# Kernel optimization log

Measured on AMD Instinct MI355X. Metric: run time of the kernel, lower is better.

The kernel has to match this reference:

```python
import jax, jax.numpy as jnp
import numpy as np

D_MODEL = 1024
NUM_HEADS = 16
HEAD_DIM = D_MODEL // NUM_HEADS


def setup_inputs() -> dict:
    key = jax.random.key(0)
    ks = jax.random.split(key, 11)
    B, S = 2, 2048
    inp = {
        "query": jax.random.normal(ks[0], (B, S, D_MODEL), jnp.float32),
        "key": jax.random.normal(ks[1], (B, S, D_MODEL), jnp.float32),
        "value": jax.random.normal(ks[2], (B, S, D_MODEL), jnp.float32),
        "mask": 1,
        "w_q": jax.random.normal(ks[3], (D_MODEL, D_MODEL), jnp.float32) / np.sqrt(D_MODEL),
        "b_q": jax.random.normal(ks[4], (D_MODEL,), jnp.float32) * 0.02,
        "w_k": jax.random.normal(ks[5], (D_MODEL, D_MODEL), jnp.float32) / np.sqrt(D_MODEL),
        "b_k": jax.random.normal(ks[6], (D_MODEL,), jnp.float32) * 0.02,
        "w_v": jax.random.normal(ks[7], (D_MODEL, D_MODEL), jnp.float32) / np.sqrt(D_MODEL),
        "b_v": jax.random.normal(ks[8], (D_MODEL,), jnp.float32) * 0.02,
        "w_o": jax.random.normal(ks[9], (D_MODEL, D_MODEL), jnp.float32) / np.sqrt(D_MODEL),
        "b_o": jax.random.normal(ks[10], (D_MODEL,), jnp.float32) * 0.02,
    }
    return inp


def reference(query, key, value, mask, w_q, b_q, w_k, b_k, w_v, b_v, w_o, b_o):
    B, S, _ = query.shape
    H, Dh = NUM_HEADS, HEAD_DIM
    # projections (torch Linear: x @ W.T + b; here w_* stored as [in, out])
    q = (query @ w_q + b_q).reshape(B, S, H, Dh).transpose(0, 2, 1, 3)  # [B,H,S,Dh]
    k = (key @ w_k + b_k).reshape(B, S, H, Dh).transpose(0, 2, 1, 3)
    v = (value @ w_v + b_v).reshape(B, S, H, Dh).transpose(0, 2, 1, 3)
    scale = 1.0 / jnp.sqrt(jnp.asarray(Dh, q.dtype))
    scores = jnp.einsum("bhqd,bhkd->bhqk", q, k) * scale  # [B,H,S,S]
    if mask:
        causal = jnp.tril(jnp.ones((S, S), dtype=bool))
        scores = jnp.where(causal, scores, jnp.asarray(-1e9, scores.dtype))
    attn = jax.nn.softmax(scores, axis=-1)
    x = jnp.einsum("bhqk,bhkd->bhqd", attn, v)  # [B,H,S,Dh]
    x = x.transpose(0, 2, 1, 3).reshape(B, S, H * Dh)
    return x @ w_o + b_o
```

## Files before the change

### kernel.cpp

```cpp
#include <hip/hip_runtime.h>
#include <hip/hip_bf16.h>

using bf16 = __hip_bfloat16;

typedef __attribute__((ext_vector_type(4))) short short4v;
typedef __attribute__((ext_vector_type(8))) short short8v;
typedef __attribute__((ext_vector_type(4))) float f32x4;

static constexpr int D  = 1024;
static constexpr int H  = 16;
static constexpr int DH = 64;
static constexpr int B  = 2;
static constexpr int S  = 2048;
static constexpr int M  = B * S;
static constexpr size_t MD = (size_t)M * D;
static constexpr size_t WSZ = (size_t)D * D;

#define QS_CONST 0.18033688011112042f

__device__ __forceinline__ unsigned short f2b(float f) {
    union { float f; unsigned u; } v; v.f = f;
    return (unsigned short)((v.u + 0x7FFFu + ((v.u >> 16) & 1u)) >> 16);
}
__device__ __forceinline__ unsigned pkbf(float a, float b) {
    float2 t; t.x = a; t.y = b;
    __hip_bfloat162 h = __float22bfloat162_rn(t);
    union { __hip_bfloat162 h; unsigned u; } cv; cv.h = h;
    return cv.u;
}
__device__ __forceinline__ short8v pack8(short4v a, short4v b) {
    short8v r;
    r[0]=a[0]; r[1]=a[1]; r[2]=a[2]; r[3]=a[3];
    r[4]=b[0]; r[5]=b[1]; r[6]=b[2]; r[7]=b[3];
    return r;
}
__device__ __forceinline__ short8v ld_frag(const short* rowp, int lg) {
    short4v a = *reinterpret_cast<const short4v*>(rowp + 4*lg);
    short4v b = *reinterpret_cast<const short4v*>(rowp + 16 + 4*lg);
    return pack8(a, b);
}

__device__ __forceinline__ void gl_lds16(const void* g, void* l) {
    __builtin_amdgcn_global_load_lds(
        (const __attribute__((address_space(1))) unsigned int*)g,
        (__attribute__((address_space(3))) unsigned int*)l, 16, 0, 0);
}

__global__ __launch_bounds__(256) void cvt_all_kernel(
    const float* __restrict__ w0, const float* __restrict__ w1,
    const float* __restrict__ w2, const float* __restrict__ w3,
    unsigned short* __restrict__ t0, unsigned short* __restrict__ t1,
    unsigned short* __restrict__ t2, unsigned short* __restrict__ t3,
    const float* __restrict__ x0, const float* __restrict__ x1,
    const float* __restrict__ x2,
    unsigned short* __restrict__ y0, unsigned short* __restrict__ y1,
    unsigned short* __restrict__ y2)
{
    __shared__ float tile[32][33];
    const int z = blockIdx.z;
    if (z < 4) {
        const float* W = z==0 ? w0 : z==1 ? w1 : z==2 ? w2 : w3;
        unsigned short* T = z==0 ? t0 : z==1 ? t1 : z==2 ? t2 : t3;
        const int k0 = (blockIdx.x & 31) * 32, n0 = (blockIdx.x >> 5) * 32;
        const int t = threadIdx.x, r = t>>3, c4 = (t&7)*4;
        float4 v = *reinterpret_cast<const float4*>(&W[(size_t)(k0+r)*D + n0 + c4]);
        tile[r][c4+0]=v.x; tile[r][c4+1]=v.y; tile[r][c4+2]=v.z; tile[r][c4+3]=v.w;
        __syncthreads();
        uint2 p;
        p.x = pkbf(tile[c4+0][r], tile[c4+1][r]);
        p.y = pkbf(tile[c4+2][r], tile[c4+3][r]);
        *reinterpret_cast<uint2*>(T + (size_t)(n0+r)*D + k0 + c4) = p;
    } else {
        const float* X = z==4 ? x0 : z==5 ? x1 : x2;
        unsigned short* Y = z==4 ? y0 : z==5 ? y1 : y2;
        const size_t base = (size_t)blockIdx.x * 256 + threadIdx.x;
        const size_t stride = (size_t)1024 * 256;
#pragma unroll
        for (int j = 0; j < 4; ++j) {
            const size_t i = base + (size_t)j * stride;
            float4 f = reinterpret_cast<const float4*>(X)[i];
            uint2 p; p.x = pkbf(f.x, f.y); p.y = pkbf(f.z, f.w);
            reinterpret_cast<uint2*>(Y)[i] = p;
        }
    }
}

#define GEMM_CORE_LDS(XPTR, WPTR)                                              \
    __shared__ short As[2][128*32];                                            \
    __shared__ short Bs[2][128*32];                                            \
    const int tid = threadIdx.x;                                               \
    const int wid = tid>>6, lane = tid&63;                                     \
    const int wr = wid>>1, wc = wid&1;                                         \
    const int lg = lane>>4, lr = lane&15;                                      \
    const int qw = (lane&3) ^ ((lane>>3)&3);        \
    const int qr = lg ^ ((lr>>1)&3);                \
    f32x4 acc[4][4];                                                           \
    _Pragma("unroll")                                                          \
    for (int i=0;i<4;i++)                                                      \
        _Pragma("unroll")                                                      \
        for (int j=0;j<4;j++) acc[i][j] = f32x4{0.f,0.f,0.f,0.f};              \
    const int srow = (lane>>2);                                                \
    auto stage = [&](int buf, int k0) {                                        \
        _Pragma("unroll")                                                      \
        for (int c=0;c<2;c++) {                                                \
            const int r0 = 32*wid + 16*c;                                      \
            const int r  = r0 + srow;                                          \
            gl_lds16(XPTR + (size_t)(m0+r)*1024 + k0 + qw*8, &As[buf][r0*32]); \
            gl_lds16(WPTR + (size_t)(n0+r)*1024 + k0 + qw*8, &Bs[buf][r0*32]); \
        }                                                                      \
    };                                                                         \
    stage(0, 0);                                                               \
    int cur = 0;                                                               \
    for (int k0 = 0; k0 < 1024; k0 += 32) {                                    \
        __syncthreads();                     \
        if (k0 + 32 < 1024) stage(cur^1, k0 + 32);                             \
        short8v af[4], bfr[4];                                                 \
        _Pragma("unroll")                                                      \
        for (int i=0;i<4;i++) {                                                \
            const int R = wr*64 + i*16 + lr;                                   \
            af[i] = *reinterpret_cast<const short8v*>(&As[cur][R*32 + qr*8]);  \
        }                                                                      \
        _Pragma("unroll")                                                      \
        for (int j=0;j<4;j++) {                                                \
            const int R = wc*64 + j*16 + lr;                                   \
            bfr[j] = *reinterpret_cast<const short8v*>(&Bs[cur][R*32 + qr*8]); \
        }                                                                      \
        __builtin_amdgcn_s_setprio(1);                                         \
        _Pragma("unroll")                                                      \
        for (int i=0;i<4;i++)                                                  \
            _Pragma("unroll")                                                  \
            for (int j=0;j<4;j++)                                              \
                acc[i][j] = __builtin_amdgcn_mfma_f32_16x16x32_bf16(           \
                    af[i], bfr[j], acc[i][j], 0,0,0);                          \
        __builtin_amdgcn_s_setprio(0);                                         \
        cur ^= 1;                                                              \
    }

__global__ __launch_bounds__(256) void gemm_qkv_lds(
    const unsigned short* __restrict__ Xq, const unsigned short* __restrict__ Xk,
    const unsigned short* __restrict__ Xv, const unsigned short* __restrict__ WtBase,
    const float* __restrict__ bq, const float* __restrict__ bk,
    const float* __restrict__ bv, unsigned short* __restrict__ qkBase,
    unsigned short* __restrict__ va)
{
    const int z = blockIdx.z;
    const unsigned short* X = z==0 ? Xq : z==1 ? Xk : Xv;
    const unsigned short* Wt = WtBase + (size_t)z * WSZ;
    const float* bias = z==0 ? bq : z==1 ? bk : bv;
    const int m0 = blockIdx.x*128, n0 = blockIdx.y*128;

    GEMM_CORE_LDS(X, Wt)

#pragma unroll
    for (int i=0;i<4;i++) {
#pragma unroll
        for (int j=0;j<4;j++) {
            const int n = n0 + wc*64 + j*16 + lr;
            const float bv2 = bias[n];
#pragma unroll
            for (int r=0;r<4;r++) {
                const int m = m0 + wr*64 + i*16 + lg*4 + r;
                float v = acc[i][j][r] + bv2;
                const int bb=m>>11, ss=m&2047, hh=n>>6, dh=n&63;
                if (z == 0) {
                    v *= QS_CONST;
                    qkBase[(((size_t)(bb*H+hh))*S + ss)*DH + dh] = f2b(v);
                } else if (z == 1) {
                    (qkBase + MD)[(((size_t)(bb*H+hh))*S + ss)*DH + dh] = f2b(v);
                } else {
                    va[(((size_t)(bb*H+hh))*DH + dh)*S + ss] = f2b(v);
                }
            }
        }
    }
}

template<int OUTBF>
__global__ __launch_bounds__(256) void gemm_out_lds(
    const unsigned short* __restrict__ Xc, const unsigned short* __restrict__ Wt,
    const float* __restrict__ bias, void* __restrict__ Y)
{
    const int m0 = blockIdx.x*128, n0 = blockIdx.y*128;

    GEMM_CORE_LDS(Xc, Wt)

#pragma unroll
    for (int i=0;i<4;i++) {
#pragma unroll
        for (int j=0;j<4;j++) {
            const int n = n0 + wc*64 + j*16 + lr;
            const float bv = bias[n];
#pragma unroll
            for (int r=0;r<4;r++) {
                const int m = m0 + wr*64 + i*16 + lg*4 + r;
                const float v = acc[i][j][r] + bv;
                if (OUTBF) ((unsigned short*)Y)[(size_t)m*D + n] = f2b(v);
                else       ((float*)Y)[(size_t)m*D + n] = v;
            }
        }
    }
}

__global__ __launch_bounds__(256) void attn_mfma(
    const unsigned short* __restrict__ Qa,
    const unsigned short* __restrict__ Ka,
    const unsigned short* __restrict__ Va,
    unsigned short* __restrict__ Ctx)
{
    __shared__ short Ks[2][64*64];
    __shared__ short Vs[2][64*64];
    short (*Ob)[72] = (short(*)[72])Ks;

    const int tid = threadIdx.x;
    const int i   = blockIdx.x;
    const int xcd = i & 7;
    const int o   = i >> 3;
    const int bh  = (xcd << 2) + (o >> 5);
    const int qt  = ((o >> 5) & 1) ? (o & 31) : 31 - (o & 31);
    const int bb = bh>>4, hh = bh&15;
    const int q0 = qt*64;
    const int wid = tid>>6, lane = tid&63;
    const int lg = lane>>4, lr = lane&15;
    const size_t qkbase = (size_t)bh*S*DH;
    const size_t vbase  = (size_t)bh*DH*S;

    const int qrow = q0 + wid*16 + lr;
    short8v qf[2];
    {
        const unsigned short* qp = Qa + qkbase + (size_t)qrow*DH;
#pragma unroll
        for (int c=0;c<2;c++) {
            short4v a = *reinterpret_cast<const short4v*>(qp + 32*c + 4*lg);
            short4v b = *reinterpret_cast<const short4v*>(qp + 32*c + 16 + 4*lg);
            qf[c] = pack8(a, b);
        }
    }

    float lsum = 0.f;
    f32x4 oacc[4];
#pragma unroll
    for (int dt=0;dt<4;dt++) oacc[dt] = f32x4{0.f,0.f,0.f,0.f};

    const int srsub = lane >> 3;
    const int scol  = 8 * ((lane & 7) ^ srsub);

    auto stage = [&](int buf, int j0) {
#pragma unroll
        for (int c2=0;c2<2;c2++) {
            const int rb = 16*wid + 8*c2;
            gl_lds16(Ka + qkbase + (size_t)(j0 + rb + srsub)*DH + scol,
                     &Ks[buf][rb*64]);
            gl_lds16(Va + vbase  + (size_t)(rb + srsub)*S + j0 + scol,
                     &Vs[buf][rb*64]);
        }
    };

    const int r7 = lr & 7;
    const int l4 = 4*(lg & 1), g0 = lg >> 1;
    int offA[2], offB[2];
#pragma unroll
    for (int c=0;c<2;c++) {
        offA[c] = l4 + 8*((4*c + g0)     ^ r7);
        offB[c] = l4 + 8*((4*c + 2 + g0) ^ r7);
    }

    const int NT = qt + 1;
    stage(0, 0);
    for (int t = 0; t < NT; ++t) {
        const int j0 = t*64;
        const int cur = t & 1;
        __syncthreads();
        if (t + 1 < NT) stage(cur ^ 1, j0 + 64);

        __builtin_amdgcn_s_setprio(1);
        f32x4 st[4];
#pragma unroll
        for (int jt=0;jt<4;jt++) {
            f32x4 s = f32x4{0.f,0.f,0.f,0.f};
#pragma unroll
            for (int c=0;c<2;c++) {
                const short* rowp = &Ks[cur][(jt*16 + lr)*64];
                short4v a = *reinterpret_cast<const short4v*>(rowp + offA[c]);
                short4v b = *reinterpret_cast<const short4v*>(rowp + offB[c]);
                s = __builtin_amdgcn_mfma_f32_16x16x32_bf16(pack8(a,b), qf[c], s, 0,0,0);
            }
            st[jt] = s;
        }
        __builtin_amdgcn_s_setprio(0);

        float p[16];
        if (t == NT-1) {
#pragma unroll
            for (int jt=0;jt<4;jt++)
#pragma unroll
                for (int r=0;r<4;r++) {
                    const int j = j0 + jt*16 + lg*4 + r;
                    p[jt*4+r] = (j <= qrow) ? st[jt][r] : -1e30f;
                }
        } else {
#pragma unroll
            for (int jt=0;jt<4;jt++)
#pragma unroll
                for (int r=0;r<4;r++) p[jt*4+r] = st[jt][r];
        }
#pragma unroll
        for (int e=0;e<16;e++) { p[e] = exp2f(p[e]); lsum += p[e]; }

        uint4 u0, u1;
        u0.x = pkbf(p[0],p[1]);   u0.y = pkbf(p[2],p[3]);
        u0.z = pkbf(p[4],p[5]);   u0.w = pkbf(p[6],p[7]);
        u1.x = pkbf(p[8],p[9]);   u1.y = pkbf(p[10],p[11]);
        u1.z = pkbf(p[12],p[13]); u1.w = pkbf(p[14],p[15]);
        short8v pf0, pf1;
        *reinterpret_cast<uint4*>(&pf0) = u0;
        *reinterpret_cast<uint4*>(&pf1) = u1;

        __builtin_amdgcn_s_setprio(1);
#pragma unroll
        for (int dt=0;dt<4;dt++) {
            const short* rowp = &Vs[cur][(dt*16 + lr)*64];
            short4v a0 = *reinterpret_cast<const short4v*>(rowp + offA[0]);
            short4v b0 = *reinterpret_cast<const short4v*>(rowp + offB[0]);
            short4v a1 = *reinterpret_cast<const short4v*>(rowp + offA[1]);
            short4v b1 = *reinterpret_cast<const short4v*>(rowp + offB[1]);
            oacc[dt] = __builtin_amdgcn_mfma_f32_16x16x32_bf16(pack8(a0,b0), pf0, oacc[dt], 0,0,0);
            oacc[dt] = __builtin_amdgcn_mfma_f32_16x16x32_bf16(pack8(a1,b1), pf1, oacc[dt], 0,0,0);
        }
        __builtin_amdgcn_s_setprio(0);
    }

    lsum += __shfl_xor(lsum, 16);
    lsum += __shfl_xor(lsum, 32);
    __syncthreads();
    const float inv = 1.f / lsum;
#pragma unroll
    for (int dt=0;dt<4;dt++) {
        uint2 w;
        w.x = pkbf(oacc[dt][0]*inv, oacc[dt][1]*inv);
        w.y = pkbf(oacc[dt][2]*inv, oacc[dt][3]*inv);
        *reinterpret_cast<uint2*>(&Ob[wid*16 + lr][dt*16 + lg*4]) = w;
    }
    __syncthreads();
    const int orow = tid>>2, oc = (tid&3)*16;
    uint4 o1 = *reinterpret_cast<const uint4*>(&Ob[orow][oc]);
    uint4 o2 = *reinterpret_cast<const uint4*>(&Ob[orow][oc+8]);
    unsigned short* dst = Ctx + ((size_t)bb*S + q0 + orow)*D + hh*DH + oc;
    *reinterpret_cast<uint4*>(dst)     = o1;
    *reinterpret_cast<uint4*>(dst + 8) = o2;
}

extern "C" void kernel_launch(void* const* d_in, const int* in_sizes, int n_in,
                              void* d_out, int out_size, void* d_ws, size_t ws_size,
                              hipStream_t stream)
{
    const float* query = (const float*)d_in[0];
    const float* key   = (const float*)d_in[1];
    const float* value = (const float*)d_in[2];
    const float* w_q = (const float*)d_in[4];
    const float* b_q = (const float*)d_in[5];
    const float* w_k = (const float*)d_in[6];
    const float* b_k = (const float*)d_in[7];
    const float* w_v = (const float*)d_in[8];
    const float* b_v = (const float*)d_in[9];
    const float* w_o = (const float*)d_in[10];
    const float* b_o = (const float*)d_in[11];

    bool out_bf16 = true;
    {
        size_t ob = 0;
        if (hipMemPtrGetInfo(d_out, &ob) == hipSuccess &&
            ob >= (size_t)out_size * 3 && ob <= (size_t)out_size * 6)
            out_bf16 = false;
    }

    unsigned short* wtq = (unsigned short*)d_ws;
    unsigned short* wtk = wtq + WSZ;
    unsigned short* wtv = wtk + WSZ;
    unsigned short* wto = wtv + WSZ;
    unsigned short* qa  = wto + WSZ;
    unsigned short* ka  = qa  + MD;
    unsigned short* va  = ka  + MD;
    unsigned short* ctx = va  + MD;
    unsigned short* xq  = ctx + MD;
    unsigned short* xk  = xq  + MD;
    unsigned short* xv  = xk  + MD;

    cvt_all_kernel<<<dim3(1024,1,7), 256, 0, stream>>>(
        w_q, w_k, w_v, w_o, wtq, wtk, wtv, wto,
        query, key, value, xq, xk, xv);

    gemm_qkv_lds<<<dim3(M/128, D/128, 3), 256, 0, stream>>>(
        xq, xk, xv, wtq, b_q, b_k, b_v, qa, va);

    attn_mfma<<<dim3((S/64) * B * H), 256, 0, stream>>>(qa, ka, va, ctx);

    if (out_bf16)
        gemm_out_lds<1><<<dim3(M/128, D/128), 256, 0, stream>>>(ctx, wto, b_o, d_out);
    else
        gemm_out_lds<0><<<dim3(M/128, D/128), 256, 0, stream>>>(ctx, wto, b_o, d_out);
}
```

Before: 134.6 us.

## Use 128-row query tiles with 8 waves and register-staged padded K/V LDS

The attention kernel now runs 512-thread blocks, each covering 128 query rows instead of 64. Each K/V tile loaded into LDS is therefore reused by twice as many query rows, which halves global K/V traffic and staging work per row. K/V staging changes from direct global-to-LDS swizzled copies to register prefetch and store into padded [64][72] LDS arrays, read back via ld_frag. The trade-offs are coarser causal load balance, fewer blocks in flight, and the loss of the async global-to-LDS copy path.

```diff
diff --git a/kernel.cpp b/kernel.cpp
--- a/kernel.cpp
+++ b/kernel.cpp
@@ -201,24 +201,24 @@
     }
 }
 
-__global__ __launch_bounds__(256) void attn_mfma(
+__global__ __launch_bounds__(512) void attn_mfma(
     const unsigned short* __restrict__ Qa,
     const unsigned short* __restrict__ Ka,
     const unsigned short* __restrict__ Va,
     unsigned short* __restrict__ Ctx)
 {
-    __shared__ short Ks[2][64*64];
-    __shared__ short Vs[2][64*64];
+    __shared__ short Ks[2][64][72];
+    __shared__ short Vs[2][64][72];
     short (*Ob)[72] = (short(*)[72])Ks;
 
     const int tid = threadIdx.x;
     const int i   = blockIdx.x;
     const int xcd = i & 7;
     const int o   = i >> 3;
-    const int bh  = (xcd << 2) + (o >> 5);
-    const int qt  = ((o >> 5) & 1) ? (o & 31) : 31 - (o & 31);
+    const int bh  = (xcd << 2) + (o >> 4);
+    const int qt  = (o < 32) ? (o & 15) : 15 - (o & 15);
     const int bb = bh>>4, hh = bh&15;
-    const int q0 = qt*64;
+    const int q0 = qt*128;
     const int wid = tid>>6, lane = tid&63;
     const int lg = lane>>4, lr = lane&15;
     const size_t qkbase = (size_t)bh*S*DH;
@@ -241,36 +241,28 @@
 #pragma unroll
     for (int dt=0;dt<4;dt++) oacc[dt] = f32x4{0.f,0.f,0.f,0.f};
 
-    const int srsub = lane >> 3;
-    const int scol  = 8 * ((lane & 7) ^ srsub);
-
-    auto stage = [&](int buf, int j0) {
-#pragma unroll
-        for (int c2=0;c2<2;c2++) {
-            const int rb = 16*wid + 8*c2;
-            gl_lds16(Ka + qkbase + (size_t)(j0 + rb + srsub)*DH + scol,
-                     &Ks[buf][rb*64]);
-            gl_lds16(Va + vbase  + (size_t)(rb + srsub)*S + j0 + scol,
-                     &Vs[buf][rb*64]);
-        }
+    const int sr = tid>>3;
+    const int sc = (tid&7)*8;
+
+    uint4 kg, vg;
+    auto load_kv = [&](int j0) {
+        kg = *reinterpret_cast<const uint4*>(Ka + qkbase + (size_t)(j0+sr)*DH + sc);
+        vg = *reinterpret_cast<const uint4*>(Va + vbase  + (size_t)sr*S + j0 + sc);
     };
-
-    const int r7 = lr & 7;
-    const int l4 = 4*(lg & 1), g0 = lg >> 1;
-    int offA[2], offB[2];
-#pragma unroll
-    for (int c=0;c<2;c++) {
-        offA[c] = l4 + 8*((4*c + g0)     ^ r7);
-        offB[c] = l4 + 8*((4*c + 2 + g0) ^ r7);
-    }
-
-    const int NT = qt + 1;
-    stage(0, 0);
+    auto store_kv = [&](int buf) {
+        *reinterpret_cast<uint4*>(&Ks[buf][sr][sc]) = kg;
+        *reinterpret_cast<uint4*>(&Vs[buf][sr][sc]) = vg;
+    };
+
+    const int NT = 2*qt + 2;
+    load_kv(0);
+    store_kv(0);
+
     for (int t = 0; t < NT; ++t) {
         const int j0 = t*64;
         const int cur = t & 1;
+        if (t + 1 < NT) load_kv(j0 + 64);
         __syncthreads();
-        if (t + 1 < NT) stage(cur ^ 1, j0 + 64);
 
         __builtin_amdgcn_s_setprio(1);
         f32x4 st[4];
@@ -279,17 +271,15 @@
             f32x4 s = f32x4{0.f,0.f,0.f,0.f};
 #pragma unroll
             for (int c=0;c<2;c++) {
-                const short* rowp = &Ks[cur][(jt*16 + lr)*64];
-                short4v a = *reinterpret_cast<const short4v*>(rowp + offA[c]);
-                short4v b = *reinterpret_cast<const short4v*>(rowp + offB[c]);
-                s = __builtin_amdgcn_mfma_f32_16x16x32_bf16(pack8(a,b), qf[c], s, 0,0,0);
+                short8v kf = ld_frag(&Ks[cur][jt*16 + lr][32*c], lg);
+                s = __builtin_amdgcn_mfma_f32_16x16x32_bf16(kf, qf[c], s, 0,0,0);
             }
             st[jt] = s;
         }
         __builtin_amdgcn_s_setprio(0);
 
         float p[16];
-        if (t == NT-1) {
+        if (t >= NT-2) {
 #pragma unroll
             for (int jt=0;jt<4;jt++)
 #pragma unroll
@@ -318,15 +308,14 @@
         __builtin_amdgcn_s_setprio(1);
 #pragma unroll
         for (int dt=0;dt<4;dt++) {
-            const short* rowp = &Vs[cur][(dt*16 + lr)*64];
-            short4v a0 = *reinterpret_cast<const short4v*>(rowp + offA[0]);
-            short4v b0 = *reinterpret_cast<const short4v*>(rowp + offB[0]);
-            short4v a1 = *reinterpret_cast<const short4v*>(rowp + offA[1]);
-            short4v b1 = *reinterpret_cast<const short4v*>(rowp + offB[1]);
-            oacc[dt] = __builtin_amdgcn_mfma_f32_16x16x32_bf16(pack8(a0,b0), pf0, oacc[dt], 0,0,0);
-            oacc[dt] = __builtin_amdgcn_mfma_f32_16x16x32_bf16(pack8(a1,b1), pf1, oacc[dt], 0,0,0);
+            short8v vf0 = ld_frag(&Vs[cur][dt*16 + lr][0],  lg);
+            short8v vf1 = ld_frag(&Vs[cur][dt*16 + lr][32], lg);
+            oacc[dt] = __builtin_amdgcn_mfma_f32_16x16x32_bf16(vf0, pf0, oacc[dt], 0,0,0);
+            oacc[dt] = __builtin_amdgcn_mfma_f32_16x16x32_bf16(vf1, pf1, oacc[dt], 0,0,0);
         }
         __builtin_amdgcn_s_setprio(0);
+
+        if (t + 1 < NT) store_kv(cur ^ 1);
     }
 
     lsum += __shfl_xor(lsum, 16);
@@ -392,7 +381,7 @@
     gemm_qkv_lds<<<dim3(M/128, D/128, 3), 256, 0, stream>>>(
         xq, xk, xv, wtq, b_q, b_k, b_v, qa, va);
 
-    attn_mfma<<<dim3((S/64) * B * H), 256, 0, stream>>>(qa, ka, va, ctx);
+    attn_mfma<<<dim3((S/128) * B * H), 512, 0, stream>>>(qa, ka, va, ctx);
 
     if (out_bf16)
         gemm_out_lds<1><<<dim3(M/128, D/128), 256, 0, stream>>>(ctx, wto, b_o, d_out);
```

After: 130.3 us. 1.03x faster.
